# Kernel tuning notes

Hardware: AMD Instinct MI355X
Metric: run time of the kernel (lower is better)

The kernel has to match this reference:

```python
import jax, jax.numpy as jnp
import numpy as np

B, N = 16, 48
NODE, EDGE, HID, MSG, LAYERS, TGT = 32, 16, 64, 64, 3, 128
NL = 128  # hidden width of cfg.net_layers / cfg.layers MLPs


def _lin(key, i, o):
    k1, k2 = jax.random.split(key)
    return (jax.random.normal(k1, (i, o), jnp.float32) * 0.05,
            jax.random.normal(k2, (o,), jnp.float32) * 0.05)


def setup_inputs() -> dict:
    key = jax.random.key(0)
    ks = jax.random.split(key, 16)
    g = (jax.random.uniform(ks[0], (B, N, N)) < 0.5).astype(jnp.float32)
    h0 = jax.random.normal(ks[1], (B, N, NODE), jnp.float32)
    e = jax.random.normal(ks[2], (B, N, N, EDGE), jnp.float32)
    msg_w0, msg_b0 = _lin(ks[3], EDGE, NL)
    msg_w1, msg_b1 = _lin(ks[4], NL, NL)
    msg_w2, msg_b2 = _lin(ks[5], NL, MSG * HID)
    gru_wih = jax.random.normal(ks[6], (3 * HID, MSG), jnp.float32) * 0.05
    gru_whh = jax.random.normal(ks[7], (3 * HID, HID), jnp.float32) * 0.05
    gru_bih = jax.random.normal(ks[8], (3 * HID,), jnp.float32) * 0.05
    gru_bhh = jax.random.normal(ks[9], (3 * HID,), jnp.float32) * 0.05
    r0_w0, r0_b0 = _lin(ks[10], 2 * HID, NL)
    r0_w1, r0_b1 = _lin(ks[11], NL, NL)
    r0_w2, r0_b2 = _lin(ks[12], NL, TGT)
    r1_w0, r1_b0 = _lin(ks[13], HID, NL)
    r1_w1, r1_b1 = _lin(ks[14], NL, NL)
    r1_w2, r1_b2 = _lin(ks[15], NL, TGT)
    return dict(g=g, h0=h0, e=e,
                msg_w0=msg_w0, msg_b0=msg_b0, msg_w1=msg_w1, msg_b1=msg_b1,
                msg_w2=msg_w2, msg_b2=msg_b2,
                gru_wih=gru_wih, gru_whh=gru_whh, gru_bih=gru_bih, gru_bhh=gru_bhh,
                r0_w0=r0_w0, r0_b0=r0_b0, r0_w1=r0_w1, r0_b1=r0_b1, r0_w2=r0_w2, r0_b2=r0_b2,
                r1_w0=r1_w0, r1_b0=r1_b0, r1_w1=r1_w1, r1_b1=r1_b1, r1_w2=r1_w2, r1_b2=r1_b2)


def _net(x, w0, b0, w1, b1, w2, b2):
    # Net: relu hidden layers, linear output (matches torch Net with 2 hidden layers)
    x = jax.nn.relu(x @ w0 + b0)
    x = jax.nn.relu(x @ w1 + b1)
    return x @ w2 + b2


def _gru_step(x, h, wih, whh, bih, bhh):
    # torch.nn.GRU single step; gate order r, z, n
    gi = x @ wih.T + bih
    gh = h @ whh.T + bhh
    r = jax.nn.sigmoid(gi[:, :HID] + gh[:, :HID])
    z = jax.nn.sigmoid(gi[:, HID:2 * HID] + gh[:, HID:2 * HID])
    n = jnp.tanh(gi[:, 2 * HID:] + r * gh[:, 2 * HID:])
    return (1.0 - z) * n + z * h


def reference(g, h0, e,
              msg_w0, msg_b0, msg_w1, msg_b1, msg_w2, msg_b2,
              gru_wih, gru_whh, gru_bih, gru_bhh,
              r0_w0, r0_b0, r0_w1, r0_b1, r0_w2, r0_b2,
              r1_w0, r1_b0, r1_w1, r1_b1, r1_w2, r1_b2):
    # pad h0 up to hidden size
    h_first = jnp.concatenate(
        [h0, jnp.zeros((B, N, HID - NODE), h0.dtype)], axis=2)
    node_mask = (jnp.sum(h0, axis=2) > 0).astype(h0.dtype)[..., None]  # [B,N,1]

    # per-edge weight matrices from edge features (same every layer in the
    # original torch code, so compute once): [B*N*N, MSG, HID]
    m_w = _net(e.reshape(-1, EDGE), msg_w0, msg_b0, msg_w1, msg_b1,
               msg_w2, msg_b2).reshape(-1, MSG, HID)

    h_t = h_first
    for _ in range(LAYERS):
        h_feat = h_t.reshape(-1, HID)  # [B*N, HID]
        # faithful to torch: expand on last dim then view(-1, HID),
        # which interleaves the hidden and neighbor axes in memory order
        h_w_rows = jnp.broadcast_to(
            h_feat[:, :, None], (B * N, HID, N)).reshape(-1, HID)
        msg = jnp.einsum('emh,eh->em', m_w, h_w_rows)  # [B*N*N, MSG]
        msg = msg.reshape(B, N, N, MSG)
        agg = jnp.sum(g[..., None] * msg, axis=1)  # masked sum over dim 1 -> [B,N,MSG]
        h_new = _gru_step(agg.reshape(-1, MSG), h_t.reshape(-1, HID),
                          gru_wih, gru_whh, gru_bih, gru_bhh).reshape(B, N, HID)
        h_t = node_mask * h_new

    # readout: Net0(cat[h_0, h_T]) * Net1(h_T), masked by h_0 activity, summed over nodes
    gate_in = jnp.concatenate([h_first, h_t], axis=-1)  # [B,N,2*HID]
    nn_res = (_net(gate_in, r0_w0, r0_b0, r0_w1, r0_b1, r0_w2, r0_b2) *
              _net(h_t, r1_w0, r1_b0, r1_w1, r1_b1, r1_w2, r1_b2))  # [B,N,TGT]
    read_mask = (jnp.sum(h_first, axis=2) > 0).astype(nn_res.dtype)[..., None]
    res = jnp.sum(read_mask * nn_res, axis=1)  # [B,TGT]
    return jax.nn.sigmoid(res)
```

## Files before the change

kernel.cpp:

```cpp
#include <hip/hip_runtime.h>
#include <cmath>

#define B_ 16
#define N_ 48
#define HID_ 64
#define NL_ 128
#define NNODE_ (B_*N_)
#define NEDGE_ (B_*N_*N_)

__device__ __forceinline__ float sigmoidf_(float x){ return 1.0f/(1.0f+expf(-x)); }

__global__ __launch_bounds__(256) void k_pm(
    const float* __restrict__ ein, const float* __restrict__ w0, const float* __restrict__ b0,
    const float* __restrict__ w1, const float* __restrict__ b1,
    const float* __restrict__ w2, const float* __restrict__ b2,
    const float* __restrict__ h0,
    const float* __restrict__ wih, const float* __restrict__ whh,
    float* __restrict__ relu2,
    float* __restrict__ A, float* __restrict__ Bm,
    float* __restrict__ Ab, float* __restrict__ Bb,
    float* __restrict__ hfirst, float* __restrict__ mask,
    float* __restrict__ wihT, float* __restrict__ whhT)
{
    __shared__ __align__(16) float x1s[64*132];
    int tid = threadIdx.x;

    if (blockIdx.x < 576){
        int et = tid & 15, ot = tid >> 4;
        int o0 = ot * 8;
        size_t e0 = (size_t)blockIdx.x * 64;

        float acc[4][8];
        {
            float4 ba = *(const float4*)&b0[o0];
            float4 bb = *(const float4*)&b0[o0 + 4];
            #pragma unroll
            for (int q = 0; q < 4; q++){
                acc[q][0]=ba.x; acc[q][1]=ba.y; acc[q][2]=ba.z; acc[q][3]=ba.w;
                acc[q][4]=bb.x; acc[q][5]=bb.y; acc[q][6]=bb.z; acc[q][7]=bb.w;
            }
        }
        #pragma unroll
        for (int i4 = 0; i4 < 4; i4++){
            float4 ev[4];
            #pragma unroll
            for (int q = 0; q < 4; q++)
                ev[q] = *(const float4*)&ein[(e0 + q*16 + et)*16 + i4*4];
            float wr[4][8];
            #pragma unroll
            for (int d = 0; d < 4; d++){
                *(float4*)&wr[d][0] = *(const float4*)&w0[(i4*4+d)*128 + o0];
                *(float4*)&wr[d][4] = *(const float4*)&w0[(i4*4+d)*128 + o0 + 4];
            }
            #pragma unroll
            for (int q = 0; q < 4; q++){
                #pragma unroll
                for (int r2 = 0; r2 < 8; r2++)
                    acc[q][r2] += ev[q].x*wr[0][r2] + ev[q].y*wr[1][r2]
                                + ev[q].z*wr[2][r2] + ev[q].w*wr[3][r2];
            }
        }
        #pragma unroll
        for (int q = 0; q < 4; q++){
            int e = q*16 + et;
            float4 s0 = make_float4(fmaxf(acc[q][0],0.f), fmaxf(acc[q][1],0.f),
                                    fmaxf(acc[q][2],0.f), fmaxf(acc[q][3],0.f));
            float4 s1 = make_float4(fmaxf(acc[q][4],0.f), fmaxf(acc[q][5],0.f),
                                    fmaxf(acc[q][6],0.f), fmaxf(acc[q][7],0.f));
            *(float4*)&x1s[e*132 + o0]     = s0;
            *(float4*)&x1s[e*132 + o0 + 4] = s1;
        }
        __syncthreads();

        float a2[4][8];
        {
            float4 ba = *(const float4*)&b1[o0];
            float4 bb = *(const float4*)&b1[o0 + 4];
            #pragma unroll
            for (int q = 0; q < 4; q++){
                a2[q][0]=ba.x; a2[q][1]=ba.y; a2[q][2]=ba.z; a2[q][3]=ba.w;
                a2[q][4]=bb.x; a2[q][5]=bb.y; a2[q][6]=bb.z; a2[q][7]=bb.w;
            }
        }
        for (int i4 = 0; i4 < 32; i4++){
            int i = i4*4;
            float wr[4][8];
            #pragma unroll
            for (int d = 0; d < 4; d++){
                *(float4*)&wr[d][0] = *(const float4*)&w1[(size_t)(i+d)*128 + o0];
                *(float4*)&wr[d][4] = *(const float4*)&w1[(size_t)(i+d)*128 + o0 + 4];
            }
            #pragma unroll
            for (int q = 0; q < 4; q++){
                float4 xv = *(const float4*)&x1s[(q*16 + et)*132 + i];
                #pragma unroll
                for (int r2 = 0; r2 < 8; r2++)
                    a2[q][r2] += xv.x*wr[0][r2] + xv.y*wr[1][r2]
                               + xv.z*wr[2][r2] + xv.w*wr[3][r2];
            }
        }
        #pragma unroll
        for (int q = 0; q < 4; q++){
            size_t e = e0 + q*16 + et;
            float4 s0 = make_float4(fmaxf(a2[q][0],0.f), fmaxf(a2[q][1],0.f),
                                    fmaxf(a2[q][2],0.f), fmaxf(a2[q][3],0.f));
            float4 s1 = make_float4(fmaxf(a2[q][4],0.f), fmaxf(a2[q][5],0.f),
                                    fmaxf(a2[q][6],0.f), fmaxf(a2[q][7],0.f));
            *(float4*)&relu2[e*128 + o0]     = s0;
            *(float4*)&relu2[e*128 + o0 + 4] = s1;
        }
    } else {
        int idx = (blockIdx.x - 576)*256 + tid;
        if (idx < 24576) {
            int r = idx >> 13, c = (idx >> 6) & 127, m = idx & 63;
            int t = 48 - 16*r;
            const float* src = w2 + c*4096 + m*64;
            float a = 0.f, b = 0.f;
            #pragma unroll
            for (int k4 = 0; k4 < 16; k4++){
                float4 v = *(const float4*)&src[k4*4];
                float s = v.x + v.y + v.z + v.w;
                if (k4*4 < t) a += s; else b += s;
            }
            A[idx] = a; Bm[idx] = b;
        } else if (idx < 24768) {
            int i2 = idx - 24576;
            int r = i2 >> 6, m = i2 & 63;
            int t = 48 - 16*r;
            const float* src = b2 + m*64;
            float a = 0.f, b = 0.f;
            #pragma unroll
            for (int k4 = 0; k4 < 16; k4++){
                float4 v = *(const float4*)&src[k4*4];
                float s = v.x + v.y + v.z + v.w;
                if (k4*4 < t) a += s; else b += s;
            }
            Ab[i2] = a; Bb[i2] = b;
        } else if (idx < 73920) {
            int i3 = idx - 24768;
            int node = i3 >> 6, m = i3 & 63;
            hfirst[i3] = (m < 32) ? h0[node*32 + m] : 0.f;
            if (m == 0) {
                float s = 0.f;
                #pragma unroll
                for (int k = 0; k < 32; k++) s += h0[node*32 + k];
                mask[node] = (s > 0.f) ? 1.f : 0.f;
            }
        } else if (idx < 98496) {
            int i4 = idx - 73920;
            if (i4 < 12288) {
                int k = i4 / 192, col = i4 - k*192;
                wihT[i4] = wih[col*64 + k];
            } else {
                int i5 = i4 - 12288;
                int k = i5 / 192, col = i5 - k*192;
                whhT[i5] = whh[col*64 + k];
            }
        }
    }
}

__global__ __launch_bounds__(256) void k_layer(
    const float* __restrict__ hin, float* __restrict__ hout,
    const float* __restrict__ relu2,
    const float* __restrict__ A, const float* __restrict__ Bm,
    const float* __restrict__ Ab, const float* __restrict__ Bb,
    const float* __restrict__ g, const float* __restrict__ mask,
    const float* __restrict__ wihT, const float* __restrict__ whhT,
    const float* __restrict__ bih, const float* __restrict__ bhh)
{
    int bj = blockIdx.x;
    int b = bj / 48, j = bj - b*48;
    int r = j % 3;
    int p0 = j + j/3;
    int tid = threadIdx.x;
    int base = b*48;
    __shared__ __align__(16) float r2s[48*128];
    __shared__ float hs[64], wAs[64], wBs[64], Abs[64], Bbs[64];
    __shared__ float pU[2][128], pV[2][128];
    __shared__ float pC[4][64];
    __shared__ float aggs[64], gi[192], gh[192];
    __shared__ float sAB[2];

    {
        const float* src = relu2 + ((size_t)base*48 + j)*128;
        #pragma unroll
        for (int q2 = 0; q2 < 6; q2++){
            int flat = q2*256 + tid;
            int row = flat >> 5, col = (flat & 31)*4;
            float4 v = *(const float4*)&src[(size_t)row*6144 + col];
            *(float4*)&r2s[row*128 + col] = v;
        }
    }
    if (tid < 64){
        hs[tid] = hin[(size_t)bj*64 + tid];
    } else if (tid < 128){
        int i = tid - 64;
        float wa = 0.f, wb = 0.f;
        if (i < 48){
            float gv = g[(size_t)(base+i)*48 + j];
            wa = gv * hin[(size_t)(base+i)*64 + p0];
            wb = gv * hin[(size_t)(base+i)*64 + p0 + 1];
        }
        wAs[i] = wa; wBs[i] = wb;
        float sa = wa, sb = wb;
        #pragma unroll
        for (int d = 32; d >= 1; d >>= 1){
            sa += __shfl_xor(sa, d, 64);
            sb += __shfl_xor(sb, d, 64);
        }
        if (i == 0){ sAB[0] = sa; sAB[1] = sb; }
    } else if (tid < 192){
        Bbs[tid-128] = Bb[r*64 + (tid-128)];
    } else {
        Abs[tid-192] = Ab[r*64 + (tid-192)];
    }
    __syncthreads();

    {
        int c = tid & 127, half = tid >> 7;
        float aU = 0.f, aV = 0.f;
        #pragma unroll
        for (int ii = 0; ii < 24; ii++){
            int i = half*24 + ii;
            float v = r2s[i*128 + c];
            aU += wAs[i]*v; aV += wBs[i]*v;
        }
        pU[half][c] = aU; pV[half][c] = aV;
    }
    __syncthreads();

    {
        int m = tid & 63, cg = tid >> 6;
        const float* Arp = A  + r*8192 + m;
        const float* Brp = Bm + r*8192 + m;
        float a = 0.f;
        #pragma unroll
        for (int cc = 0; cc < 32; cc++){
            int c = cg*32 + cc;
            float u = pU[0][c] + pU[1][c];
            float v = pV[0][c] + pV[1][c];
            a += u*Arp[(size_t)c*64] + v*Brp[(size_t)c*64];
        }
        pC[cg][m] = a;
    }
    __syncthreads();

    if (tid < 64){
        aggs[tid] = pC[0][tid] + pC[1][tid] + pC[2][tid] + pC[3][tid]
                  + sAB[0]*Abs[tid] + sAB[1]*Bbs[tid];
    }
    __syncthreads();

    if (tid < 192){
        float gacc = bih[tid], hacc = bhh[tid];
        #pragma unroll 16
        for (int k = 0; k < 64; k++){
            gacc += aggs[k] * wihT[k*192 + tid];
            hacc += hs[k]   * whhT[k*192 + tid];
        }
        gi[tid] = gacc; gh[tid] = hacc;
    }
    __syncthreads();

    if (tid < 64){
        float rr = sigmoidf_(gi[tid] + gh[tid]);
        float zz = sigmoidf_(gi[64+tid] + gh[64+tid]);
        float nn = tanhf(gi[128+tid] + rr*gh[128+tid]);
        float hnew = (1.f - zz)*nn + zz*hs[tid];
        hout[(size_t)bj*64 + tid] = mask[bj] * hnew;
    }
}

__device__ __forceinline__ void stage_w(const float* __restrict__ W,
                                        float* __restrict__ Ws, int rows, int tid)
{
    for (int f = tid; f < rows*32; f += 256){
        int i = f >> 5, c4 = (f & 31) << 2;
        *(float4*)&Ws[i*129 + c4] = *(const float4*)&W[(size_t)i*128 + c4];
    }
}

__device__ __forceinline__ void lds_layer(const float* __restrict__ Ws,
    const float* __restrict__ xsrc,
    const float* __restrict__ bias, float* __restrict__ dst,
    int dim, int o, int ng, bool do_relu)
{
    float a0 = bias[o];
    float a1 = a0;
    #pragma unroll 8
    for (int k = 0; k < dim; k += 4){
        float4 x0 = *(const float4*)&xsrc[ng*132 + k];
        float4 x1 = *(const float4*)&xsrc[(ng+2)*132 + k];
        float w0 = Ws[(k+0)*129 + o];
        float w1 = Ws[(k+1)*129 + o];
        float w2 = Ws[(k+2)*129 + o];
        float w3 = Ws[(k+3)*129 + o];
        a0 += x0.x*w0 + x0.y*w1 + x0.z*w2 + x0.w*w3;
        a1 += x1.x*w0 + x1.y*w1 + x1.z*w2 + x1.w*w3;
    }
    if (do_relu){ a0 = fmaxf(a0, 0.f); a1 = fmaxf(a1, 0.f); }
    dst[ng*132 + o] = a0;
    dst[(ng+2)*132 + o] = a1;
}

__global__ __launch_bounds__(256) void k_read(
    const float* __restrict__ hfirst, const float* __restrict__ hT,
    const float* __restrict__ mask,
    const float* __restrict__ w00, const float* __restrict__ b00,
    const float* __restrict__ w01, const float* __restrict__ b01,
    const float* __restrict__ w02, const float* __restrict__ b02,
    const float* __restrict__ w10, const float* __restrict__ b10,
    const float* __restrict__ w11, const float* __restrict__ b11,
    const float* __restrict__ w12, const float* __restrict__ b12,
    float* __restrict__ partial)
{
    __shared__ __align__(16) float Ws[128*129];
    __shared__ __align__(16) float xs[4*132], ys[4*132], zs[4*132], os0[4*132];
    __shared__ float mS[4];
    int tid = threadIdx.x;
    int b = blockIdx.x / 12, gg = blockIdx.x - b*12;
    int node0 = b*48 + gg*4;
    int o = tid & 127, ng = tid >> 7;

    if (tid < 4) mS[tid] = mask[node0 + tid];
    for (int i = tid; i < 4*128; i += 256){
        int r = i >> 7, c = i & 127;
        xs[r*132 + c] = (c < 64) ? hfirst[(size_t)(node0+r)*64 + c]
                                 : hT[(size_t)(node0+r)*64 + (c - 64)];
    }
    stage_w(w00, Ws, 128, tid);                       __syncthreads();
    lds_layer(Ws, xs,      b00, ys,  128, o, ng, true);  __syncthreads();
    stage_w(w01, Ws, 128, tid);                       __syncthreads();
    lds_layer(Ws, ys,      b01, zs,  128, o, ng, true);  __syncthreads();
    stage_w(w02, Ws, 128, tid);                       __syncthreads();
    lds_layer(Ws, zs,      b02, os0, 128, o, ng, false); __syncthreads();
    stage_w(w10, Ws, 64, tid);                        __syncthreads();
    lds_layer(Ws, xs + 64, b10, ys,  64,  o, ng, true);  __syncthreads();
    stage_w(w11, Ws, 128, tid);                       __syncthreads();
    lds_layer(Ws, ys,      b11, zs,  128, o, ng, true);  __syncthreads();
    stage_w(w12, Ws, 128, tid);                       __syncthreads();
    {
        float a0 = b12[o];
        float a1 = a0;
        #pragma unroll 8
        for (int k = 0; k < 128; k += 4){
            float4 x0 = *(const float4*)&zs[ng*132 + k];
            float4 x1 = *(const float4*)&zs[(ng+2)*132 + k];
            float w0 = Ws[(k+0)*129 + o];
            float w1 = Ws[(k+1)*129 + o];
            float w2 = Ws[(k+2)*129 + o];
            float w3 = Ws[(k+3)*129 + o];
            a0 += x0.x*w0 + x0.y*w1 + x0.z*w2 + x0.w*w3;
            a1 += x1.x*w0 + x1.y*w1 + x1.z*w2 + x1.w*w3;
        }
        float s = mS[ng]   * os0[ng*132 + o]     * a0
                + mS[ng+2] * os0[(ng+2)*132 + o] * a1;
        __syncthreads();
        ys[ng*132 + o] = s;
    }
    __syncthreads();
    if (tid < 128)
        partial[(size_t)blockIdx.x*128 + tid] = ys[tid] + ys[132 + tid];
}

__global__ void k_final(const float* __restrict__ partial, float* __restrict__ out)
{
    int idx = blockIdx.x*256 + threadIdx.x;
    if (idx < B_*128){
        int b = idx >> 7, t = idx & 127;
        float s = 0.f;
        #pragma unroll
        for (int c = 0; c < 12; c++) s += partial[(size_t)(b*12 + c)*128 + t];
        out[idx] = 1.0f / (1.0f + expf(-s));
    }
}

extern "C" void kernel_launch(void* const* d_in, const int* in_sizes, int n_in,
                              void* d_out, int out_size, void* d_ws, size_t ws_size,
                              hipStream_t stream)
{
    (void)in_sizes; (void)n_in; (void)out_size; (void)ws_size;
    const float* g    = (const float*)d_in[0];
    const float* h0   = (const float*)d_in[1];
    const float* e    = (const float*)d_in[2];
    const float* mw0  = (const float*)d_in[3];
    const float* mb0  = (const float*)d_in[4];
    const float* mw1  = (const float*)d_in[5];
    const float* mb1  = (const float*)d_in[6];
    const float* mw2  = (const float*)d_in[7];
    const float* mb2  = (const float*)d_in[8];
    const float* wih  = (const float*)d_in[9];
    const float* whh  = (const float*)d_in[10];
    const float* bih  = (const float*)d_in[11];
    const float* bhh  = (const float*)d_in[12];
    const float* r0w0 = (const float*)d_in[13];
    const float* r0b0 = (const float*)d_in[14];
    const float* r0w1 = (const float*)d_in[15];
    const float* r0b1 = (const float*)d_in[16];
    const float* r0w2 = (const float*)d_in[17];
    const float* r0b2 = (const float*)d_in[18];
    const float* r1w0 = (const float*)d_in[19];
    const float* r1b0 = (const float*)d_in[20];
    const float* r1w1 = (const float*)d_in[21];
    const float* r1b1 = (const float*)d_in[22];
    const float* r1w2 = (const float*)d_in[23];
    const float* r1b2 = (const float*)d_in[24];
    float* out = (float*)d_out;

    float* ws     = (float*)d_ws;
    float* A      = ws;
    float* Bm     = A      + 24576;
    float* Ab     = Bm     + 24576;
    float* Bb     = Ab     + 192;
    float* hfirst = Bb     + 192;
    float* hA     = hfirst + 49152;
    float* hB     = hA     + 49152;
    float* mask   = hB     + 49152;
    float* wihT   = mask   + 768;
    float* whhT   = wihT   + 12288;
    float* part   = whhT   + 12288;
    float* relu2  = part   + 24576;

    k_pm<<<961, 256, 0, stream>>>(e, mw0, mb0, mw1, mb1, mw2, mb2, h0, wih, whh,
                                  relu2, A, Bm, Ab, Bb, hfirst, mask, wihT, whhT);
    k_layer<<<768, 256, 0, stream>>>(hfirst, hA, relu2, A, Bm, Ab, Bb, g, mask,
                                     wihT, whhT, bih, bhh);
    k_layer<<<768, 256, 0, stream>>>(hA, hB, relu2, A, Bm, Ab, Bb, g, mask,
                                     wihT, whhT, bih, bhh);
    k_layer<<<768, 256, 0, stream>>>(hB, hA, relu2, A, Bm, Ab, Bb, g, mask,
                                     wihT, whhT, bih, bhh);
    k_read<<<192, 256, 0, stream>>>(hfirst, hA, mask,
                                    r0w0, r0b0, r0w1, r0b1, r0w2, r0b2,
                                    r1w0, r1b0, r1w1, r1b1, r1w2, r1b2, part);
    k_final<<<8, 256, 0, stream>>>(part, out);
}
```

Before: 206.1 us.

## Fuse three message-passing layers into one persistent kernel per graph

Replaces three launches of a 768-block per-node layer kernel with one 16-block, 1024-thread kernel. Each block owns one graph and loops over all three layers in shared memory, computing hidden-to-hidden GRU terms alongside the message aggregation. This removes two launches, the round trips of hidden state through global memory, and the per-node re-reading of weights. The cost is only 16 blocks on a GPU with many compute units, so parallelism drops sharply and each block now reads the whole relu2 slab serially. It also adds a launch-bounds occupancy hint to the readout kernel.

```diff
diff --git a/kernel.cpp b/kernel.cpp
--- a/kernel.cpp
+++ b/kernel.cpp
@@ -160,8 +160,8 @@
     }
 }
 
-__global__ __launch_bounds__(256) void k_layer(
-    const float* __restrict__ hin, float* __restrict__ hout,
+__global__ __launch_bounds__(1024) void k_layers(
+    const float* __restrict__ hfirst, float* __restrict__ hT,
     const float* __restrict__ relu2,
     const float* __restrict__ A, const float* __restrict__ Bm,
     const float* __restrict__ Ab, const float* __restrict__ Bb,
@@ -169,106 +169,173 @@
     const float* __restrict__ wihT, const float* __restrict__ whhT,
     const float* __restrict__ bih, const float* __restrict__ bhh)
 {
-    int bj = blockIdx.x;
-    int b = bj / 48, j = bj - b*48;
-    int r = j % 3;
-    int p0 = j + j/3;
-    int tid = threadIdx.x;
-    int base = b*48;
-    __shared__ __align__(16) float r2s[48*128];
-    __shared__ float hs[64], wAs[64], wBs[64], Abs[64], Bbs[64];
-    __shared__ float pU[2][128], pV[2][128];
-    __shared__ float pC[4][64];
-    __shared__ float aggs[64], gi[192], gh[192];
-    __shared__ float sAB[2];
-
-    {
-        const float* src = relu2 + ((size_t)base*48 + j)*128;
-        #pragma unroll
-        for (int q2 = 0; q2 < 6; q2++){
-            int flat = q2*256 + tid;
-            int row = flat >> 5, col = (flat & 31)*4;
-            float4 v = *(const float4*)&src[(size_t)row*6144 + col];
-            *(float4*)&r2s[row*128 + col] = v;
-        }
-    }
-    if (tid < 64){
-        hs[tid] = hin[(size_t)bj*64 + tid];
-    } else if (tid < 128){
-        int i = tid - 64;
-        float wa = 0.f, wb = 0.f;
-        if (i < 48){
-            float gv = g[(size_t)(base+i)*48 + j];
-            wa = gv * hin[(size_t)(base+i)*64 + p0];
-            wb = gv * hin[(size_t)(base+i)*64 + p0 + 1];
-        }
-        wAs[i] = wa; wBs[i] = wb;
-        float sa = wa, sb = wb;
-        #pragma unroll
-        for (int d = 32; d >= 1; d >>= 1){
-            sa += __shfl_xor(sa, d, 64);
-            sb += __shfl_xor(sb, d, 64);
-        }
-        if (i == 0){ sAB[0] = sa; sAB[1] = sb; }
-    } else if (tid < 192){
-        Bbs[tid-128] = Bb[r*64 + (tid-128)];
-    } else {
-        Abs[tid-192] = Ab[r*64 + (tid-192)];
-    }
+    __shared__ float hs[3072];
+    __shared__ float wAs[48*49], wBs[48*49];
+    __shared__ __align__(16) float scr[12288];
+    __shared__ float aggS[3072];
+    __shared__ float ghS[9216];
+    __shared__ float sA[48], sB[48], mkS[48];
+
+    const int b = blockIdx.x, base = b*48;
+    const int tid = threadIdx.x;
+    float* U = scr;
+    float* V = scr + 6144;
+
+    for (int t = tid; t < 3072; t += 1024) hs[t] = hfirst[(size_t)base*64 + t];
+    if (tid < 48) mkS[tid] = mask[base + tid];
     __syncthreads();
 
-    {
-        int c = tid & 127, half = tid >> 7;
-        float aU = 0.f, aV = 0.f;
-        #pragma unroll
-        for (int ii = 0; ii < 24; ii++){
-            int i = half*24 + ii;
-            float v = r2s[i*128 + c];
-            aU += wAs[i]*v; aV += wBs[i]*v;
-        }
-        pU[half][c] = aU; pV[half][c] = aV;
-    }
-    __syncthreads();
-
-    {
-        int m = tid & 63, cg = tid >> 6;
-        const float* Arp = A  + r*8192 + m;
-        const float* Brp = Bm + r*8192 + m;
-        float a = 0.f;
-        #pragma unroll
-        for (int cc = 0; cc < 32; cc++){
-            int c = cg*32 + cc;
-            float u = pU[0][c] + pU[1][c];
-            float v = pV[0][c] + pV[1][c];
-            a += u*Arp[(size_t)c*64] + v*Brp[(size_t)c*64];
-        }
-        pC[cg][m] = a;
-    }
-    __syncthreads();
-
-    if (tid < 64){
-        aggs[tid] = pC[0][tid] + pC[1][tid] + pC[2][tid] + pC[3][tid]
-                  + sAB[0]*Abs[tid] + sAB[1]*Bbs[tid];
-    }
-    __syncthreads();
-
-    if (tid < 192){
-        float gacc = bih[tid], hacc = bhh[tid];
-        #pragma unroll 16
-        for (int k = 0; k < 64; k++){
-            gacc += aggs[k] * wihT[k*192 + tid];
-            hacc += hs[k]   * whhT[k*192 + tid];
-        }
-        gi[tid] = gacc; gh[tid] = hacc;
-    }
-    __syncthreads();
-
-    if (tid < 64){
-        float rr = sigmoidf_(gi[tid] + gh[tid]);
-        float zz = sigmoidf_(gi[64+tid] + gh[64+tid]);
-        float nn = tanhf(gi[128+tid] + rr*gh[128+tid]);
-        float hnew = (1.f - zz)*nn + zz*hs[tid];
-        hout[(size_t)bj*64 + tid] = mask[bj] * hnew;
+    for (int L = 0; L < 3; L++){
+        #pragma unroll
+        for (int rd = 0; rd < 3; rd++){
+            int t = rd*1024 + tid;
+            if (t < 2304){
+                int i = t / 48, j = t - i*48;
+                int p0 = j + j/3;
+                float gv = g[(size_t)(base+i)*48 + j];
+                wAs[i*49+j] = gv * hs[i*64 + p0];
+                wBs[i*49+j] = gv * hs[i*64 + p0 + 1];
+            }
+            aggS[t] = 0.f;
+        }
+        __syncthreads();
+        if (tid < 48){
+            float s = 0.f;
+            #pragma unroll
+            for (int i = 0; i < 48; i++) s += wAs[i*49+tid];
+            sA[tid] = s;
+        } else if (tid >= 64 && tid < 112){
+            int j = tid - 64;
+            float s = 0.f;
+            #pragma unroll
+            for (int i = 0; i < 48; i++) s += wBs[i*49+j];
+            sB[j] = s;
+        }
+        __syncthreads();
+
+        if (tid < 768){
+            #pragma unroll
+            for (int p = 0; p < 2; p++){
+                int pt = p*768 + tid;
+                int j = pt >> 5, c4 = (pt & 31) << 2;
+                const float* src = relu2 + ((size_t)base*48 + j)*128 + c4;
+                float4 aU = make_float4(0.f,0.f,0.f,0.f);
+                float4 aV = make_float4(0.f,0.f,0.f,0.f);
+                #pragma unroll 8
+                for (int i = 0; i < 48; i++){
+                    float4 v = *(const float4*)&src[(size_t)i*6144];
+                    float wa = wAs[i*49+j], wb = wBs[i*49+j];
+                    aU.x += wa*v.x; aU.y += wa*v.y; aU.z += wa*v.z; aU.w += wa*v.w;
+                    aV.x += wb*v.x; aV.y += wb*v.y; aV.z += wb*v.z; aV.w += wb*v.w;
+                }
+                *(float4*)&U[j*128 + c4] = aU;
+                *(float4*)&V[j*128 + c4] = aV;
+            }
+        } else {
+            int t2 = tid - 768;
+            int og = t2 & 63, q = t2 >> 6;
+            float ar[12], az[12], an[12];
+            {
+                float b0v = bhh[og], b1v = bhh[64+og], b2v = bhh[128+og];
+                #pragma unroll
+                for (int t16 = 0; t16 < 12; t16++){ ar[t16]=b0v; az[t16]=b1v; an[t16]=b2v; }
+            }
+            #pragma unroll 2
+            for (int k = 0; k < 64; k++){
+                float w0v = whhT[k*192 + og];
+                float w1v = whhT[k*192 + 64 + og];
+                float w2v = whhT[k*192 + 128 + og];
+                #pragma unroll
+                for (int t16 = 0; t16 < 12; t16++){
+                    float h = hs[(q*12 + t16)*64 + k];
+                    ar[t16] += h*w0v; az[t16] += h*w1v; an[t16] += h*w2v;
+                }
+            }
+            #pragma unroll
+            for (int t16 = 0; t16 < 12; t16++){
+                int j = q*12 + t16;
+                ghS[j*192 + og]       = ar[t16];
+                ghS[j*192 + 64 + og]  = az[t16];
+                ghS[j*192 + 128 + og] = an[t16];
+            }
+        }
+        __syncthreads();
+
+        {
+            int m = tid & 63, cq = tid >> 6;
+            #pragma unroll
+            for (int rr = 0; rr < 3; rr++){
+                float acc[16];
+                #pragma unroll
+                for (int t16 = 0; t16 < 16; t16++) acc[t16] = 0.f;
+                #pragma unroll
+                for (int cc = 0; cc < 8; cc++){
+                    int c = cq*8 + cc;
+                    float av = A [rr*8192 + c*64 + m];
+                    float bv = Bm[rr*8192 + c*64 + m];
+                    #pragma unroll
+                    for (int t16 = 0; t16 < 16; t16++){
+                        int j = rr + 3*t16;
+                        acc[t16] += U[j*128 + c]*av + V[j*128 + c]*bv;
+                    }
+                }
+                #pragma unroll
+                for (int t16 = 0; t16 < 16; t16++)
+                    atomicAdd(&aggS[(rr + 3*t16)*64 + m], acc[t16]);
+            }
+        }
+        __syncthreads();
+        #pragma unroll
+        for (int rd = 0; rd < 3; rd++){
+            int t = rd*1024 + tid;
+            int j = t >> 6, m = t & 63, r = j % 3;
+            aggS[t] += sA[j]*Ab[r*64 + m] + sB[j]*Bb[r*64 + m];
+        }
+        __syncthreads();
+
+        #pragma unroll
+        for (int q4 = 0; q4 < 3; q4++){
+            int f = q4*1024 + tid;
+            *(float4*)&scr[f*4] = *(const float4*)&wihT[(size_t)f*4];
+        }
+        __syncthreads();
+        {
+            int og = tid & 63, jp = tid >> 6;
+            float gr[3], gz[3], gn[3];
+            {
+                float bi0 = bih[og], bi1 = bih[64+og], bi2 = bih[128+og];
+                #pragma unroll
+                for (int d = 0; d < 3; d++){ gr[d]=bi0; gz[d]=bi1; gn[d]=bi2; }
+            }
+            #pragma unroll 2
+            for (int k = 0; k < 64; k++){
+                float w0v = scr[k*192 + og];
+                float w1v = scr[k*192 + 64 + og];
+                float w2v = scr[k*192 + 128 + og];
+                #pragma unroll
+                for (int d = 0; d < 3; d++){
+                    float a = aggS[(jp*3 + d)*64 + k];
+                    gr[d] += a*w0v; gz[d] += a*w1v; gn[d] += a*w2v;
+                }
+            }
+            float hnew[3];
+            #pragma unroll
+            for (int d = 0; d < 3; d++){
+                int j = jp*3 + d;
+                float rr_ = sigmoidf_(gr[d] + ghS[j*192 + og]);
+                float zz  = sigmoidf_(gz[d] + ghS[j*192 + 64 + og]);
+                float nn  = tanhf(gn[d] + rr_*ghS[j*192 + 128 + og]);
+                hnew[d] = mkS[j]*((1.f - zz)*nn + zz*hs[j*64 + og]);
+            }
+            __syncthreads();
+            #pragma unroll
+            for (int d = 0; d < 3; d++){
+                int j = jp*3 + d;
+                hs[j*64 + og] = hnew[d];
+                if (L == 2) hT[(size_t)(base + j)*64 + og] = hnew[d];
+            }
+        }
+        __syncthreads();
     }
 }
 
@@ -304,7 +371,7 @@
     dst[(ng+2)*132 + o] = a1;
 }
 
-__global__ __launch_bounds__(256) void k_read(
+__global__ __launch_bounds__(256, 2) void k_read(
     const float* __restrict__ hfirst, const float* __restrict__ hT,
     const float* __restrict__ mask,
     const float* __restrict__ w00, const float* __restrict__ b00,
@@ -415,8 +482,7 @@
     float* Bb     = Ab     + 192;
     float* hfirst = Bb     + 192;
     float* hA     = hfirst + 49152;
-    float* hB     = hA     + 49152;
-    float* mask   = hB     + 49152;
+    float* mask   = hA     + 49152;
     float* wihT   = mask   + 768;
     float* whhT   = wihT   + 12288;
     float* part   = whhT   + 12288;
@@ -424,12 +490,8 @@
 
     k_pm<<<961, 256, 0, stream>>>(e, mw0, mb0, mw1, mb1, mw2, mb2, h0, wih, whh,
                                   relu2, A, Bm, Ab, Bb, hfirst, mask, wihT, whhT);
-    k_layer<<<768, 256, 0, stream>>>(hfirst, hA, relu2, A, Bm, Ab, Bb, g, mask,
-                                     wihT, whhT, bih, bhh);
-    k_layer<<<768, 256, 0, stream>>>(hA, hB, relu2, A, Bm, Ab, Bb, g, mask,
-                                     wihT, whhT, bih, bhh);
-    k_layer<<<768, 256, 0, stream>>>(hB, hA, relu2, A, Bm, Ab, Bb, g, mask,
-                                     wihT, whhT, bih, bhh);
+    k_layers<<<16, 1024, 0, stream>>>(hfirst, hA, relu2, A, Bm, Ab, Bb,
+                                      g, mask, wihT, whhT, bih, bhh);
     k_read<<<192, 256, 0, stream>>>(hfirst, hA, mask,
                                     r0w0, r0b0, r0w1, r0b1, r0w2, r0b2,
                                     r1w0, r1b0, r1w1, r1b1, r1w2, r1b2, part);
```

Measured after the change: 591.8 us. 187% more time.
